# Kernel optimization log

Hardware: AMD Instinct MI355X
Metric: run time of the kernel (lower is better)

## Reference

```python
import jax, jax.numpy as jnp
import numpy as np
from jax import lax

NUM_OBJECTS = 3
KERNEL_DIM = 3
REDUCTION = 8


def setup_inputs() -> dict:
    key = jax.random.key(0)
    k1, k2, k3 = jax.random.split(key, 3)
    bs, C, h, w = 8, 256, 64, 64
    steps = 3
    f_e = jax.random.normal(k1, (bs, C, h, w), dtype=jnp.float32)
    # [steps, num_objects*k*k, bs, emb_dim]
    all_prototypes = jax.random.normal(k2, (steps, NUM_OBJECTS * KERNEL_DIM * KERNEL_DIM, bs, C), dtype=jnp.float32) * 0.05
    w_head = jax.random.normal(k3, (C,), dtype=jnp.float32) * 0.05
    b_head = jnp.zeros((1,), dtype=jnp.float32)
    return {"f_e": f_e, "all_prototypes": all_prototypes, "w_head": w_head, "b_head": b_head}


def reference(f_e, all_prototypes, w_head, b_head):
    bs, C, h, w = f_e.shape
    steps = all_prototypes.shape[0]
    no, k = NUM_OBJECTS, KERNEL_DIM
    pad = k // 2
    # tile f_e over objects -> single-batch multi-channel input, [1, bs*no*C, h, w]
    lhs = jnp.broadcast_to(f_e[:, None], (bs, no, C, h, w)).reshape(1, bs * no * C, h, w)
    groups = bs * no * C
    outs = []
    for i in range(steps):  # small fixed loop over iterative OPE steps
        # [no*k*k, bs, C] -> [bs, no, C, k, k]
        protos = (all_prototypes[i]
                  .transpose(1, 0, 2)
                  .reshape(bs, no, k, k, C)
                  .transpose(0, 1, 4, 2, 3))
        rhs = protos.reshape(groups, 1, k, k)
        # depthwise correlation, groups = bs*no*C (matches F.conv2d with groups)
        resp = lax.conv_general_dilated(
            lhs, rhs, window_strides=(1, 1), padding=[(pad, pad), (pad, pad)],
            feature_group_count=groups,
            dimension_numbers=("NCHW", "OIHW", "NCHW"),
        ).reshape(bs, no, C, h, w)
        # softmax over object axis, then softmax-weighted sum over objects
        sm = jax.nn.softmax(resp, axis=1)
        reduced = jnp.sum(sm * resp, axis=1)  # [bs, C, h, w]
        dmap = jax.nn.relu(jnp.einsum("bchw,c->bhw", reduced, w_head) + b_head[0])[:, None]
        up = jax.image.resize(dmap, (bs, 1, h * REDUCTION, w * REDUCTION), method="bilinear")
        outs.append(up)
    return jnp.stack(outs)  # [steps, bs, 1, H, W]; outs[-1] is final, rest aux
```

## Files before the change

### kernel.cpp

```cpp
#include <hip/hip_runtime.h>
#include <math.h>

#define STEPS 3
#define BS 8
#define NCH 256
#define H 64
#define W 64
#define UP 8
#define OH (H*UP)
#define OW (W*UP)
#define GB 16
#define CPB (NCH/GB)
#define CPW (CPB/4)
#define WREC 32
#define DMAP_FLOATS (STEPS*BS*H*W)
#define PREP_N (STEPS*28*BS*NCH)

__global__ __launch_bounds__(256) void loca_prep(
    const float* __restrict__ ap, const float* __restrict__ w_head,
    float* __restrict__ wt)
{
    int t = blockIdx.x * 256 + threadIdx.x;
    if (t >= PREP_N) return;
    int c = t & (NCH - 1);
    int r = t >> 8;
    int b = r & (BS - 1);
    r >>= 3;
    int j = r % 28;
    int i = r / 28;
    float v = (j < 27) ? ap[(((size_t)i * 27 + j) * BS + b) * NCH + c] : w_head[c];
    wt[(((size_t)b * NCH + c) * STEPS + i) * WREC + j] = v;
}

__global__ __launch_bounds__(256) void loca_dmap(
    const float* __restrict__ f_e,
    const float* __restrict__ wt,
    float* __restrict__ partial)
{
    __shared__ float wlds[CPB * STEPS * WREC];
    __shared__ float red[4][STEPS][256];

    const int tid  = threadIdx.x;
    const int lane = tid & 63;
    const int wv   = tid >> 6;
    const int rb   = blockIdx.x;
    const int b    = blockIdx.y;
    const int g    = blockIdx.z;
    const int row  = rb * 4 + (lane >> 4);
    const int xg   = lane & 15;
    const int C0   = g * CPB;

    {
        const float4* src = (const float4*)(wt + ((size_t)b * NCH + C0) * (STEPS * WREC));
        float4* dst = (float4*)wlds;
        dst[tid] = src[tid];
        if (tid < CPB * STEPS * WREC / 4 - 256)
            dst[256 + tid] = src[256 + tid];
    }
    __syncthreads();

    const float m_m1 = (row > 0)     ? 1.f : 0.f;
    const float m_p1 = (row < H - 1) ? 1.f : 0.f;
    const int r_m1 = row > 0     ? row - 1 : 0;
    const int r_p1 = row < H - 1 ? row + 1 : H - 1;

    const int cw = C0 + wv * CPW;
    const float* fb = f_e + ((size_t)b * NCH + cw) * (H * W);

    float acc[STEPS][4] = {};

    float4 nm = ((const float4*)(fb + r_m1 * W))[xg];
    float4 n0 = ((const float4*)(fb + row  * W))[xg];
    float4 np = ((const float4*)(fb + r_p1 * W))[xg];

    for (int cc = 0; cc < CPW; ++cc) {
        float4 vm = nm, v0 = n0, vp = np;
        if (cc + 1 < CPW) {
            const float* fc = fb + (cc + 1) * (H * W);
            nm = ((const float4*)(fc + r_m1 * W))[xg];
            n0 = ((const float4*)(fc + row  * W))[xg];
            np = ((const float4*)(fc + r_p1 * W))[xg];
        }
        vm.x *= m_m1; vm.y *= m_m1; vm.z *= m_m1; vm.w *= m_m1;
        vp.x *= m_p1; vp.y *= m_p1; vp.z *= m_p1; vp.w *= m_p1;

        float Lm = __shfl_up(vm.w, 1);
        float L0 = __shfl_up(v0.w, 1);
        float Lp = __shfl_up(vp.w, 1);
        float Rm = __shfl_down(vm.x, 1);
        float R0 = __shfl_down(v0.x, 1);
        float Rp = __shfl_down(vp.x, 1);
        if (xg == 0)  { Lm = 0.f; L0 = 0.f; Lp = 0.f; }
        if (xg == 15) { Rm = 0.f; R0 = 0.f; Rp = 0.f; }

        float am[6]  = {Lm, vm.x, vm.y, vm.z, vm.w, Rm};
        float a0[6]  = {L0, v0.x, v0.y, v0.z, v0.w, R0};
        float apv[6] = {Lp, vp.x, vp.y, vp.z, vp.w, Rp};

        const int lc = wv * CPW + cc;

        #pragma unroll
        for (int i = 0; i < STEPS; ++i) {
            union { float4 v4[7]; float f[28]; } qq;
            const float4* wp4 = (const float4*)(wlds + ((size_t)lc * STEPS + i) * WREC);
            #pragma unroll
            for (int q = 0; q < 7; ++q) qq.v4[q] = wp4[q];
            const float wh = qq.f[27];

            #pragma unroll
            for (int k = 0; k < 4; ++k) {
                float r_[3];
                #pragma unroll
                for (int o = 0; o < 3; ++o) {
                    float t = am[k] * qq.f[o * 9 + 0];
                    t = fmaf(am[k+1],  qq.f[o * 9 + 1], t);
                    t = fmaf(am[k+2],  qq.f[o * 9 + 2], t);
                    t = fmaf(a0[k],    qq.f[o * 9 + 3], t);
                    t = fmaf(a0[k+1],  qq.f[o * 9 + 4], t);
                    t = fmaf(a0[k+2],  qq.f[o * 9 + 5], t);
                    t = fmaf(apv[k],   qq.f[o * 9 + 6], t);
                    t = fmaf(apv[k+1], qq.f[o * 9 + 7], t);
                    t = fmaf(apv[k+2], qq.f[o * 9 + 8], t);
                    r_[o] = t;
                }
                float mx = fmaxf(r_[0], fmaxf(r_[1], r_[2]));
                float e0 = __expf(r_[0] - mx);
                float e1 = __expf(r_[1] - mx);
                float e2 = __expf(r_[2] - mx);
                float num = fmaf(e0, r_[0], fmaf(e1, r_[1], e2 * r_[2]));
                float den = e0 + e1 + e2;
#if __has_builtin(__builtin_amdgcn_rcpf)
                float redv = num * __builtin_amdgcn_rcpf(den);
#else
                float redv = num / den;
#endif
                acc[i][k] = fmaf(wh, redv, acc[i][k]);
            }
        }
    }

    const int px = (lane >> 4) * 64 + xg * 4;
    #pragma unroll
    for (int i = 0; i < STEPS; ++i) {
        float4 a; a.x = acc[i][0]; a.y = acc[i][1]; a.z = acc[i][2]; a.w = acc[i][3];
        *(float4*)&red[wv][i][px] = a;
    }
    __syncthreads();
    #pragma unroll
    for (int i = 0; i < STEPS; ++i) {
        float4 s0 = *(const float4*)&red[0][i][px];
        float4 s1 = *(const float4*)&red[1][i][px];
        float4 s2 = *(const float4*)&red[2][i][px];
        float4 s3 = *(const float4*)&red[3][i][px];
        float4 s;
        s.x = (s0.x + s1.x) + (s2.x + s3.x);
        s.y = (s0.y + s1.y) + (s2.y + s3.y);
        s.z = (s0.z + s1.z) + (s2.z + s3.z);
        s.w = (s0.w + s1.w) + (s2.w + s3.w);
        *(float4*)&partial[(size_t)g * DMAP_FLOATS + ((size_t)(i * BS + b)) * (H * W)
                           + row * W + xg * 4] = s;
    }
}

__global__ __launch_bounds__(256) void loca_reduce(
    const float* __restrict__ partial, const float* __restrict__ b_head,
    float* __restrict__ dmap)
{
    const int t = blockIdx.x * 256 + threadIdx.x;
    const float4* p = (const float4*)partial;
    float4 s = p[t];
    #pragma unroll
    for (int g = 1; g < GB; ++g) {
        float4 q = p[(size_t)g * (DMAP_FLOATS / 4) + t];
        s.x += q.x; s.y += q.y; s.z += q.z; s.w += q.w;
    }
    const float bias = b_head[0];
    s.x = fmaxf(s.x + bias, 0.f);
    s.y = fmaxf(s.y + bias, 0.f);
    s.z = fmaxf(s.z + bias, 0.f);
    s.w = fmaxf(s.w + bias, 0.f);
    ((float4*)dmap)[t] = s;
}

__global__ __launch_bounds__(256) void loca_upsample(
    const float* __restrict__ dmap, float* __restrict__ out)
{
    const int idx  = blockIdx.x * 256 + threadIdx.x;
    const int gx   = idx & (OW / 4 - 1);
    const int rest = idx >> 7;
    const int Y    = rest & (OH - 1);
    const int ib   = rest >> 9;

    const float* d = dmap + (size_t)ib * H * W;

    float yin = (Y + 0.5f) * 0.125f - 0.5f;
    float fy0 = floorf(yin);
    int   iy  = (int)fy0;
    float fy  = yin - fy0;
    int y0c = min(max(iy, 0), H - 1);
    int y1c = min(max(iy + 1, 0), H - 1);
    const float* row0 = d + y0c * W;
    const float* row1 = d + y1c * W;

    float4 o;
    float* op = &o.x;
    #pragma unroll
    for (int j = 0; j < 4; ++j) {
        int X = gx * 4 + j;
        float xin = (X + 0.5f) * 0.125f - 0.5f;
        float fx0 = floorf(xin);
        int   ix  = (int)fx0;
        float fx  = xin - fx0;
        int x0c = min(max(ix, 0), W - 1);
        int x1c = min(max(ix + 1, 0), W - 1);
        float a00 = row0[x0c], a01 = row0[x1c];
        float a10 = row1[x0c], a11 = row1[x1c];
        float v0 = a00 + fx * (a01 - a00);
        float v1 = a10 + fx * (a11 - a10);
        op[j] = v0 + fy * (v1 - v0);
    }
    ((float4*)out)[idx] = o;
}

extern "C" void kernel_launch(void* const* d_in, const int* in_sizes, int n_in,
                              void* d_out, int out_size, void* d_ws, size_t ws_size,
                              hipStream_t stream) {
    const float* f_e    = (const float*)d_in[0];
    const float* ap     = (const float*)d_in[1];
    const float* w_head = (const float*)d_in[2];
    const float* b_head = (const float*)d_in[3];
    float* out  = (float*)d_out;
    float* dmap = (float*)d_ws;
    float* wt   = dmap + DMAP_FLOATS;
    float* partial = out;

    loca_prep<<<(PREP_N + 255) / 256, 256, 0, stream>>>(ap, w_head, wt);

    dim3 g1(16, BS, GB);
    loca_dmap<<<g1, 256, 0, stream>>>(f_e, wt, partial);

    loca_reduce<<<DMAP_FLOATS / 4 / 256, 256, 0, stream>>>(partial, b_head, dmap);

    const int groups = STEPS * BS * OH * OW / 4;
    loca_upsample<<<groups / 256, 256, 0, stream>>>(dmap, out);
}
```

Before: 121.4 us.

## Fuse partial reduction with bilinear upsample and halve channel-group split

Measured after the change: 116.3 us. -4.2%, faster.

```diff
diff --git a/kernel.cpp b/kernel.cpp
--- a/kernel.cpp
+++ b/kernel.cpp
@@ -9,7 +9,7 @@
 #define UP 8
 #define OH (H*UP)
 #define OW (W*UP)
-#define GB 16
+#define GB 8
 #define CPB (NCH/GB)
 #define CPW (CPB/4)
 #define WREC 32
@@ -32,7 +32,7 @@
     wt[(((size_t)b * NCH + c) * STEPS + i) * WREC + j] = v;
 }
 
-__global__ __launch_bounds__(256) void loca_dmap(
+__global__ __launch_bounds__(256, 4) void loca_dmap(
     const float* __restrict__ f_e,
     const float* __restrict__ wt,
     float* __restrict__ partial)
@@ -53,9 +53,9 @@
     {
         const float4* src = (const float4*)(wt + ((size_t)b * NCH + C0) * (STEPS * WREC));
         float4* dst = (float4*)wlds;
-        dst[tid] = src[tid];
-        if (tid < CPB * STEPS * WREC / 4 - 256)
-            dst[256 + tid] = src[256 + tid];
+        dst[tid]       = src[tid];
+        dst[256 + tid] = src[256 + tid];
+        dst[512 + tid] = src[512 + tid];
     }
     __syncthreads();
 
@@ -162,64 +162,63 @@
     }
 }
 
-__global__ __launch_bounds__(256) void loca_reduce(
-    const float* __restrict__ partial, const float* __restrict__ b_head,
-    float* __restrict__ dmap)
+__global__ __launch_bounds__(256) void loca_upred(
+    const float* __restrict__ partial,
+    const float* __restrict__ b_head,
+    float* __restrict__ out)
 {
-    const int t = blockIdx.x * 256 + threadIdx.x;
-    const float4* p = (const float4*)partial;
-    float4 s = p[t];
+    __shared__ float sm[3][W];
+
+    const int k  = blockIdx.x;
+    const int ib = blockIdx.y;
+    const int t  = threadIdx.x;
+
+    if (t < 3 * W) {
+        const int r  = t >> 6;
+        const int x  = t & (W - 1);
+        int ry = k - 1 + r;
+        ry = min(max(ry, 0), H - 1);
+        const float* p = partial + (size_t)ib * (H * W) + (size_t)ry * W + x;
+        float s = 0.f;
+        #pragma unroll
+        for (int g = 0; g < GB; ++g) s += p[(size_t)g * DMAP_FLOATS];
+        sm[r][x] = fmaxf(s + b_head[0], 0.f);
+    }
+    __syncthreads();
+
+    float* obase = out + (size_t)ib * (OH * OW) + (size_t)(UP * k) * OW;
     #pragma unroll
-    for (int g = 1; g < GB; ++g) {
-        float4 q = p[(size_t)g * (DMAP_FLOATS / 4) + t];
-        s.x += q.x; s.y += q.y; s.z += q.z; s.w += q.w;
-    }
-    const float bias = b_head[0];
-    s.x = fmaxf(s.x + bias, 0.f);
-    s.y = fmaxf(s.y + bias, 0.f);
-    s.z = fmaxf(s.z + bias, 0.f);
-    s.w = fmaxf(s.w + bias, 0.f);
-    ((float4*)dmap)[t] = s;
-}
-
-__global__ __launch_bounds__(256) void loca_upsample(
-    const float* __restrict__ dmap, float* __restrict__ out)
-{
-    const int idx  = blockIdx.x * 256 + threadIdx.x;
-    const int gx   = idx & (OW / 4 - 1);
-    const int rest = idx >> 7;
-    const int Y    = rest & (OH - 1);
-    const int ib   = rest >> 9;
-
-    const float* d = dmap + (size_t)ib * H * W;
-
-    float yin = (Y + 0.5f) * 0.125f - 0.5f;
-    float fy0 = floorf(yin);
-    int   iy  = (int)fy0;
-    float fy  = yin - fy0;
-    int y0c = min(max(iy, 0), H - 1);
-    int y1c = min(max(iy + 1, 0), H - 1);
-    const float* row0 = d + y0c * W;
-    const float* row1 = d + y1c * W;
-
-    float4 o;
-    float* op = &o.x;
-    #pragma unroll
-    for (int j = 0; j < 4; ++j) {
-        int X = gx * 4 + j;
-        float xin = (X + 0.5f) * 0.125f - 0.5f;
-        float fx0 = floorf(xin);
-        int   ix  = (int)fx0;
-        float fx  = xin - fx0;
-        int x0c = min(max(ix, 0), W - 1);
-        int x1c = min(max(ix + 1, 0), W - 1);
-        float a00 = row0[x0c], a01 = row0[x1c];
-        float a10 = row1[x0c], a11 = row1[x1c];
-        float v0 = a00 + fx * (a01 - a00);
-        float v1 = a10 + fx * (a11 - a10);
-        op[j] = v0 + fy * (v1 - v0);
-    }
-    ((float4*)out)[idx] = o;
+    for (int rep = 0; rep < 4; ++rep) {
+        const int u  = rep * 256 + t;
+        const int ry = u >> 7;
+        const int gx = u & 127;
+
+        float yin = (UP * k + ry + 0.5f) * 0.125f - 0.5f;
+        float fy0 = floorf(yin);
+        int   iy  = (int)fy0;
+        float fy  = yin - fy0;
+        const float* r0 = sm[iy - (k - 1)];
+        const float* r1 = sm[iy - (k - 1) + 1];
+
+        float4 o;
+        float* op = &o.x;
+        #pragma unroll
+        for (int j = 0; j < 4; ++j) {
+            int X = gx * 4 + j;
+            float xin = (X + 0.5f) * 0.125f - 0.5f;
+            float fx0 = floorf(xin);
+            int   ix  = (int)fx0;
+            float fx  = xin - fx0;
+            int x0c = min(max(ix, 0), W - 1);
+            int x1c = min(max(ix + 1, 0), W - 1);
+            float a00 = r0[x0c], a01 = r0[x1c];
+            float a10 = r1[x0c], a11 = r1[x1c];
+            float v0 = a00 + fx * (a01 - a00);
+            float v1 = a10 + fx * (a11 - a10);
+            op[j] = v0 + fy * (v1 - v0);
+        }
+        ((float4*)obase)[u] = o;
+    }
 }
 
 extern "C" void kernel_launch(void* const* d_in, const int* in_sizes, int n_in,
@@ -229,18 +228,15 @@
     const float* ap     = (const float*)d_in[1];
     const float* w_head = (const float*)d_in[2];
     const float* b_head = (const float*)d_in[3];
-    float* out  = (float*)d_out;
-    float* dmap = (float*)d_ws;
-    float* wt   = dmap + DMAP_FLOATS;
-    float* partial = out;
+    float* out     = (float*)d_out;
+    float* wt      = (float*)d_ws;
+    float* partial = wt + (size_t)BS * NCH * STEPS * WREC;
 
     loca_prep<<<(PREP_N + 255) / 256, 256, 0, stream>>>(ap, w_head, wt);
 
     dim3 g1(16, BS, GB);
     loca_dmap<<<g1, 256, 0, stream>>>(f_e, wt, partial);
 
-    loca_reduce<<<DMAP_FLOATS / 4 / 256, 256, 0, stream>>>(partial, b_head, dmap);
-
-    const int groups = STEPS * BS * OH * OW / 4;
-    loca_upsample<<<groups / 256, 256, 0, stream>>>(dmap, out);
-}
+    dim3 g2(H, STEPS * BS);
+    loca_upred<<<g2, 256, 0, stream>>>(partial, b_head, out);
+}
```
